# Kernel optimization log

Hardware: AMD Instinct MI355X
Metric: run time of the kernel (lower is better)

The kernel has to match this reference:

```python
import jax, jax.numpy as jnp
import numpy as np


def setup_inputs() -> dict:
    key = jax.random.key(0)
    ks = jax.random.split(key, 8)
    B, C, H, W = 4, 512, 64, 64
    Cq = C // 8
    s = 1.0 / np.sqrt(C)
    return {
        "x": jax.random.normal(ks[0], (B, C, H, W), jnp.float32),
        "Wq": jax.random.normal(ks[1], (Cq, C), jnp.float32) * s,
        "bq": jax.random.normal(ks[2], (Cq,), jnp.float32) * 0.01,
        "Wk": jax.random.normal(ks[3], (Cq, C), jnp.float32) * s,
        "bk": jax.random.normal(ks[4], (Cq,), jnp.float32) * 0.01,
        "Wv": jax.random.normal(ks[5], (C, C), jnp.float32) * s,
        "bv": jax.random.normal(ks[6], (C,), jnp.float32) * 0.01,
        "gamma": jax.random.normal(ks[7], (1,), jnp.float32),
    }


def reference(x, Wq, bq, Wk, bk, Wv, bv, gamma):
    B, C, H, W = x.shape
    N = H * W
    xf = x.reshape(B, C, N)  # flatten spatial; 1x1 conv == channel matmul
    q = jnp.einsum('oc,bcn->bon', Wq, xf) + bq[None, :, None]  # [B, C/8, N]
    k = jnp.einsum('oc,bcn->bon', Wk, xf) + bk[None, :, None]  # [B, C/8, N]
    v = jnp.einsum('oc,bcn->bon', Wv, xf) + bv[None, :, None]  # [B, C, N]
    energy = jnp.einsum('bdi,bdj->bij', q, k)                  # [B, N, N] (no scaling, as original)
    attention = jax.nn.softmax(energy, axis=-1)
    out = jnp.einsum('bcj,bij->bci', v, attention)             # bmm(v, att^T)
    out = out.reshape(B, C, H, W)
    return gamma[0] * out + x
```

## Files before the change

kernel.cpp:

```cpp
#include <hip/hip_runtime.h>


typedef float    f32x2 __attribute__((ext_vector_type(2)));
typedef float    f32x4 __attribute__((ext_vector_type(4)));
typedef _Float16 f16x4 __attribute__((ext_vector_type(4)));
typedef _Float16 f16x8 __attribute__((ext_vector_type(8)));
typedef short    bf16x8 __attribute__((ext_vector_type(8)));
typedef unsigned short u16x8 __attribute__((ext_vector_type(8)));

#define MFMA_F16(a, b, c)  __builtin_amdgcn_mfma_f32_16x16x32_f16((a), (b), (c), 0, 0, 0)
#define MFMA_BF16(a, b, c) __builtin_amdgcn_mfma_f32_16x16x32_bf16((a), (b), (c), 0, 0, 0)

__device__ __forceinline__ unsigned short bf16_rne(float f) {
    unsigned u = __builtin_bit_cast(unsigned, f);
    u += 0x7FFFu + ((u >> 16) & 1u);
    return (unsigned short)(u >> 16);
}
__device__ __forceinline__ float bf16_f(unsigned short h) {
    unsigned u = (unsigned)h << 16;
    return __builtin_bit_cast(float, u);
}

__device__ __forceinline__ void gload_lds16(const void* g, void* l) {
    __builtin_amdgcn_global_load_lds(
        (const __attribute__((address_space(1))) unsigned int*)g,
        (__attribute__((address_space(3))) unsigned int*)l, 16, 0, 0);
}

#define BARRIER_LGKM() do {                                   \
    asm volatile("s_waitcnt lgkmcnt(0)" ::: "memory");        \
    __builtin_amdgcn_s_barrier();                             \
    asm volatile("" ::: "memory");                            \
} while (0)

#define VM_WAIT8() do {                                       \
    asm volatile("s_waitcnt vmcnt(8)" ::: "memory");          \
    __builtin_amdgcn_sched_barrier(0);                        \
} while (0)
#define VM_WAIT0() do {                                       \
    asm volatile("s_waitcnt vmcnt(0)" ::: "memory");          \
    __builtin_amdgcn_sched_barrier(0);                        \
} while (0)

constexpr int BB = 4, CCH = 512, NS = 4096;

__global__ void prep_kernel(
    const float* __restrict__ Wq, const float* __restrict__ Wk,
    const float* __restrict__ Wv,
    _Float16* __restrict__ Wqh, _Float16* __restrict__ Wkh,
    _Float16* __restrict__ Wvh)
{
    const int idx = blockIdx.x * 256 + threadIdx.x;
    {
        f32x4 v = *(const f32x4*)&Wv[(size_t)idx * 4];
        f16x4 o;
#pragma unroll
        for (int e = 0; e < 4; ++e) o[e] = (_Float16)v[e];
        *(f16x4*)&Wvh[(size_t)idx * 4] = o;
    }
    if (idx < 8192) {
        f32x4 q = *(const f32x4*)&Wq[(size_t)idx * 4];
        f32x4 k = *(const f32x4*)&Wk[(size_t)idx * 4];
        f16x4 qo, ko;
#pragma unroll
        for (int e = 0; e < 4; ++e) { qo[e] = (_Float16)q[e]; ko[e] = (_Float16)k[e]; }
        *(f16x4*)&Wqh[(size_t)idx * 4] = qo;
        *(f16x4*)&Wkh[(size_t)idx * 4] = ko;
    }
}

__global__ __launch_bounds__(512, 4) void proj_kernel(
    const float* __restrict__ x,
    const _Float16* __restrict__ Wqh, const _Float16* __restrict__ Wkh,
    const _Float16* __restrict__ Wvh,
    const float* __restrict__ bq, const float* __restrict__ bk,
    const float* __restrict__ bv,
    _Float16* __restrict__ qws, _Float16* __restrict__ kws,
    unsigned short* __restrict__ vws)
{
    const int t = threadIdx.x, lane = t & 63, w = t >> 6;
    const int l15 = lane & 15, l4 = lane >> 4;
    const int b  = blockIdx.x >> 7;
    const int n0 = (blockIdx.x & 127) * 32;
    const float* xb = x + (size_t)b * CCH * NS;

    __shared__ _Float16 xt[32][32];

    f32x4 accv[4][2];
    f32x4 accq[2];
#pragma unroll
    for (int a = 0; a < 4; ++a)
#pragma unroll
        for (int n = 0; n < 2; ++n)
#pragma unroll
            for (int r = 0; r < 4; ++r) accv[a][n][r] = 0.f;
#pragma unroll
    for (int n = 0; n < 2; ++n)
#pragma unroll
        for (int r = 0; r < 4; ++r) accq[n][r] = 0.f;

    const _Float16* Wh = (w < 4) ? Wqh : Wkh;
    const int oq0 = (w & 3) * 16;
    const int stg_c = t >> 4;
    const int stg_n = (t & 15) * 2;

    f32x2 xv = *(const f32x2*)&xb[(size_t)stg_c * NS + n0 + stg_n];

    for (int cc = 0; cc < 16; ++cc) {
#pragma unroll
        for (int u = 0; u < 2; ++u) {
            const int row = stg_n + u;
            const int bcol = stg_c * 2;
            const int sw = (((bcol >> 4) ^ (row & 3)) << 4) | (bcol & 15);
            *(_Float16*)((char*)&xt[0][0] + row * 64 + sw) = (_Float16)xv[u];
        }
        BARRIER_LGKM();

        f16x8 bh[2];
#pragma unroll
        for (int nf = 0; nf < 2; ++nf) {
            const int r = nf * 16 + l15;
            bh[nf] = *(const f16x8*)((char*)&xt[0][0] + r * 64 + ((l4 ^ (r & 3)) << 4));
        }
        const int c8 = cc * 32 + l4 * 8;

        const int ccn = (cc + 1) & 15;
        xv = *(const f32x2*)&xb[(size_t)(ccn * 32 + stg_c) * NS + n0 + stg_n];

#pragma unroll
        for (int af = 0; af < 4; ++af) {
            f16x8 ah = *(const f16x8*)&Wvh[(size_t)(w * 64 + af * 16 + l15) * CCH + c8];
#pragma unroll
            for (int nf = 0; nf < 2; ++nf)
                accv[af][nf] = MFMA_F16(ah, bh[nf], accv[af][nf]);
        }
        {
            f16x8 ah = *(const f16x8*)&Wh[(size_t)(oq0 + l15) * CCH + c8];
#pragma unroll
            for (int nf = 0; nf < 2; ++nf)
                accq[nf] = MFMA_F16(ah, bh[nf], accq[nf]);
        }
        BARRIER_LGKM();
    }

#pragma unroll
    for (int af = 0; af < 4; ++af) {
#pragma unroll
        for (int r = 0; r < 4; ++r) {
            const int o = w * 64 + af * 16 + l4 * 4 + r;
            const float bias = bv[o];
#pragma unroll
            for (int nf = 0; nf < 2; ++nf) {
                const int n = n0 + nf * 16 + l15;
                vws[(size_t)(b * CCH + o) * NS + n] = bf16_rne(accv[af][nf][r] + bias);
            }
        }
    }
    {
        _Float16* oT = (w < 4) ? qws : kws;
        const float* bqk = (w < 4) ? bq : bk;
        float bias[4];
#pragma unroll
        for (int r = 0; r < 4; ++r) bias[r] = bqk[oq0 + l4 * 4 + r];
#pragma unroll
        for (int nf = 0; nf < 2; ++nf) {
            const int n = n0 + nf * 16 + l15;
            f16x4 hv;
#pragma unroll
            for (int r = 0; r < 4; ++r) hv[r] = (_Float16)(accq[nf][r] + bias[r]);
            *(f16x4*)&oT[((size_t)(b * NS + n)) * 64 + oq0 + l4 * 4] = hv;
        }
    }
}

__global__ __launch_bounds__(256, 4) void qk_kernel(
    const _Float16* __restrict__ qws, const _Float16* __restrict__ kws,
    unsigned short* __restrict__ Pws, float* __restrict__ lws2, int b0)
{
    const int t = threadIdx.x, lane = t & 63, w = t >> 6;
    const int l15 = lane & 15, l4 = lane >> 4;
    const int pb = blockIdx.x >> 8;
    const int b  = b0 + pb;
    const int r255 = blockIdx.x & 255;
    const int i0 = (r255 >> 1) * 32;
    const int jh = r255 & 1;
    const int jbase = jh * 2048;

    __shared__ unsigned short Pt[2][32][128];

    f16x8 qa[2][2];
#pragma unroll
    for (int f = 0; f < 2; ++f)
#pragma unroll
        for (int ds = 0; ds < 2; ++ds)
            qa[f][ds] = *(const f16x8*)&qws[((size_t)(b * NS + i0 + f * 16 + l15)) * 64 + ds * 32 + l4 * 8];

    const _Float16* kb = kws + (size_t)b * NS * 64;
    f16x8 kf[2][2];
#pragma unroll
    for (int jf = 0; jf < 2; ++jf)
#pragma unroll
        for (int ds = 0; ds < 2; ++ds)
            kf[jf][ds] = *(const f16x8*)&kb[(size_t)(jbase + w * 32 + jf * 16 + l15) * 64 + ds * 32 + l4 * 8];

    const int wrow = t >> 3, wg = t & 7;
    const int offA = wrow * 256 + ((wg       ^ (wrow & 7)) * 16);
    const int offB = wrow * 256 + (((wg + 8) ^ (wrow & 7)) * 16);
    unsigned short* Pgrow = Pws + ((size_t)pb * NS + i0 + wrow) * NS + jbase;
    float lacc = 0.f;

    for (int jt = 0; jt < 16; ++jt) {
        const int buf = jt & 1;
        f32x4 e[2][2];
#pragma unroll
        for (int f = 0; f < 2; ++f)
#pragma unroll
            for (int jf = 0; jf < 2; ++jf)
#pragma unroll
                for (int r = 0; r < 4; ++r) e[f][jf][r] = 0.f;
#pragma unroll
        for (int ds = 0; ds < 2; ++ds)
#pragma unroll
            for (int f = 0; f < 2; ++f)
#pragma unroll
                for (int jf = 0; jf < 2; ++jf)
                    e[f][jf] = MFMA_F16(qa[f][ds], kf[jf][ds], e[f][jf]);

        const int jn = jbase + (((jt + 1) & 15) * 128);
#pragma unroll
        for (int jf = 0; jf < 2; ++jf)
#pragma unroll
            for (int ds = 0; ds < 2; ++ds)
                kf[jf][ds] = *(const f16x8*)&kb[(size_t)(jn + w * 32 + jf * 16 + l15) * 64 + ds * 32 + l4 * 8];

        char* pbase = (char*)&Pt[buf][0][0];
#pragma unroll
        for (int f = 0; f < 2; ++f)
#pragma unroll
            for (int jf = 0; jf < 2; ++jf) {
                const int col = w * 32 + jf * 16 + l15;
#pragma unroll
                for (int r = 0; r < 4; ++r) {
                    const int row = f * 16 + l4 * 4 + r;
                    const unsigned short us = bf16_rne(__expf(e[f][jf][r]));
                    *(unsigned short*)(pbase + row * 256 +
                        (((col >> 3) ^ (row & 7)) * 16) + (col & 7) * 2) = us;
                }
            }
        BARRIER_LGKM();

        {
            char* base = (char*)&Pt[buf][0][0];
            u16x8 va = *(const u16x8*)(base + offA);
            u16x8 vb = *(const u16x8*)(base + offB);
#pragma unroll
            for (int e2 = 0; e2 < 8; ++e2)
                lacc += bf16_f((unsigned short)va[e2]) + bf16_f((unsigned short)vb[e2]);
            *(u16x8*)&Pgrow[jt * 128 + wg * 8]      = va;
            *(u16x8*)&Pgrow[jt * 128 + wg * 8 + 64] = vb;
        }
    }

    lacc += __shfl_xor(lacc, 1);
    lacc += __shfl_xor(lacc, 2);
    lacc += __shfl_xor(lacc, 4);
    if (wg == 0) lws2[((size_t)jh * BB + b) * NS + i0 + wrow] = lacc;
}

__global__ __launch_bounds__(256, 2) void pv_kernel(
    const unsigned short* __restrict__ Pws, const unsigned short* __restrict__ vws,
    const float* __restrict__ lws2, const float* __restrict__ x,
    const float* __restrict__ gamma, float* __restrict__ out, int b0, int cpx)
{
    const int t = threadIdx.x, lane = t & 63, w = t >> 6;
    const int l15 = lane & 15, l4 = lane >> 4;
    const int bid = (int)blockIdx.x;
    const int swzid = (bid & 7) * cpx + (bid >> 3);
    const int pb = swzid >> 7;
    const int b  = b0 + pb;
    const int r7 = swzid & 127;
    const int in = r7 >> 2, cm = r7 & 3;
    const int wr = w >> 1, wc = w & 1;

    __shared__ unsigned short Vt[2][128][64];
    __shared__ unsigned short Pt2[2][128][64];

    const int srow = w * 8 + (lane >> 3);
    const int sg   = (lane & 7) ^ (srow & 7);
    const unsigned short* gV = vws + ((size_t)(b * CCH + cm * 128 + srow)) * NS + sg * 8;
    const unsigned short* gP = Pws + ((size_t)(pb * NS + in * 128 + srow)) * NS + sg * 8;

    f32x4 acc[4][4];
#pragma unroll
    for (int m = 0; m < 4; ++m)
#pragma unroll
        for (int n = 0; n < 4; ++n)
#pragma unroll
            for (int r = 0; r < 4; ++r) acc[m][n][r] = 0.f;

    int offa[2][4], offb[2][4];
#pragma unroll
    for (int kk = 0; kk < 2; ++kk) {
        const int g = (kk * 4 + l4) ^ (l15 & 7);
#pragma unroll
        for (int m = 0; m < 4; ++m) {
            offa[kk][m] = (wr * 64 + m * 16 + l15) * 128 + g * 16;
            offb[kk][m] = (wc * 64 + m * 16 + l15) * 128 + g * 16;
        }
    }

#define PV_STAGE(kt, buf) do {                                                  \
    const unsigned short* _gV = gV + (size_t)(kt) * 64;                         \
    const unsigned short* _gP = gP + (size_t)(kt) * 64;                         \
    char* _lV = (char*)&Vt[buf][0][0]  + w * 1024;                              \
    char* _lP = (char*)&Pt2[buf][0][0] + w * 1024;                              \
    _Pragma("unroll")                                                           \
    for (int q = 0; q < 4; ++q) {                                               \
        gload_lds16(_gV + (size_t)q * 32 * NS, _lV + q * 4096);                 \
        gload_lds16(_gP + (size_t)q * 32 * NS, _lP + q * 4096);                 \
    }                                                                           \
} while (0)

#define PV_COMPUTE(buf) do {                                                    \
    __builtin_amdgcn_s_setprio(1);                                              \
    _Pragma("unroll")                                                           \
    for (int kk = 0; kk < 2; ++kk) {                                            \
        bf16x8 a[4], bfr[4];                                                    \
        _Pragma("unroll")                                                       \
        for (int m = 0; m < 4; ++m) {                                           \
            a[m]   = *(const bf16x8*)((char*)&Vt[buf][0][0]  + offa[kk][m]);    \
            bfr[m] = *(const bf16x8*)((char*)&Pt2[buf][0][0] + offb[kk][m]);    \
        }                                                                       \
        _Pragma("unroll")                                                       \
        for (int m = 0; m < 4; ++m)                                             \
            _Pragma("unroll")                                                   \
            for (int n = 0; n < 4; ++n)                                         \
                acc[m][n] = MFMA_BF16(a[m], bfr[n], acc[m][n]);                 \
    }                                                                           \
    __builtin_amdgcn_s_setprio(0);                                              \
} while (0)

    PV_STAGE(0, 0);
    for (int kt = 0; kt < 62; kt += 2) {
        PV_STAGE(kt + 1, 1);
        VM_WAIT8();
        __builtin_amdgcn_s_barrier();
        PV_COMPUTE(0);
        BARRIER_LGKM();
        PV_STAGE(kt + 2, 0);
        VM_WAIT8();
        __builtin_amdgcn_s_barrier();
        PV_COMPUTE(1);
        BARRIER_LGKM();
    }
    PV_STAGE(63, 1);
    VM_WAIT8();
    __builtin_amdgcn_s_barrier();
    PV_COMPUTE(0);
    BARRIER_LGKM();
    VM_WAIT0();
    __builtin_amdgcn_s_barrier();
    PV_COMPUTE(1);

#undef PV_STAGE
#undef PV_COMPUTE

    const float gm = gamma[0];
    float linv[4];
#pragma unroll
    for (int n = 0; n < 4; ++n) {
        const int i = in * 128 + wc * 64 + n * 16 + l15;
        linv[n] = 1.f / (lws2[(size_t)b * NS + i] +
                         lws2[((size_t)BB + b) * NS + i]);
    }
#pragma unroll
    for (int m = 0; m < 4; ++m) {
#pragma unroll
        for (int r = 0; r < 4; ++r) {
            const int c = cm * 128 + wr * 64 + m * 16 + l4 * 4 + r;
            const float* xr = x + ((size_t)(b * CCH + c)) * NS;
            float* orow = out + ((size_t)(b * CCH + c)) * NS;
#pragma unroll
            for (int n = 0; n < 4; ++n) {
                const int i = in * 128 + wc * 64 + n * 16 + l15;
                orow[i] = gm * acc[m][n][r] * linv[n] + xr[i];
            }
        }
    }
}

extern "C" void kernel_launch(void* const* d_in, const int* in_sizes, int n_in,
                              void* d_out, int out_size, void* d_ws, size_t ws_size,
                              hipStream_t stream)
{
    const float* x     = (const float*)d_in[0];
    const float* Wq    = (const float*)d_in[1];
    const float* bq    = (const float*)d_in[2];
    const float* Wk    = (const float*)d_in[3];
    const float* bk    = (const float*)d_in[4];
    const float* Wv    = (const float*)d_in[5];
    const float* bv    = (const float*)d_in[6];
    const float* gamma = (const float*)d_in[7];
    float* out = (float*)d_out;

    char* p = (char*)d_ws;
    size_t off = 0;
    auto take = [&](size_t bytes) { char* r = p + off; off += (bytes + 255) & ~(size_t)255; return r; };
    _Float16* qws       = (_Float16*)take((size_t)BB * NS * 64 * 2);
    _Float16* kws       = (_Float16*)take((size_t)BB * NS * 64 * 2);
    unsigned short* vws = (unsigned short*)take((size_t)BB * CCH * NS * 2);
    _Float16* Wvh       = (_Float16*)take((size_t)CCH * CCH * 2);
    _Float16* Wqh       = (_Float16*)take((size_t)64 * CCH * 2);
    _Float16* Wkh       = (_Float16*)take((size_t)64 * CCH * 2);
    float* lws2         = (float*)take((size_t)2 * BB * NS * 4);
    unsigned short* Pws = (unsigned short*)(p + off);

    const size_t P_PER_B = (size_t)NS * NS * 2;
    size_t avail = (ws_size > off) ? (ws_size - off) : 0;
    int nb = (int)(avail / P_PER_B);
    if (nb >= 4) nb = 4; else if (nb >= 2) nb = 2; else nb = 1;

    prep_kernel<<<256, 256, 0, stream>>>(Wq, Wk, Wv, Wqh, Wkh, Wvh);
    proj_kernel<<<512, 512, 0, stream>>>(x, Wqh, Wkh, Wvh, bq, bk, bv,
                                         qws, kws, vws);
    for (int b0 = 0; b0 < BB; b0 += nb) {
        const int nbb = (b0 + nb <= BB) ? nb : (BB - b0);
        qk_kernel<<<nbb * 256, 256, 0, stream>>>(qws, kws, Pws, lws2, b0);
        pv_kernel<<<nbb * 128, 256, 0, stream>>>(Pws, vws, lws2, x, gamma, out,
                                                 b0, (nbb * 128) >> 3);
    }
}
```

Baseline: 163.7 us.

## Double-buffer projection staging and make QK tile writes per-wave without block barriers

```diff
diff --git a/kernel.cpp b/kernel.cpp
--- a/kernel.cpp
+++ b/kernel.cpp
@@ -84,7 +84,7 @@
     const int n0 = (blockIdx.x & 127) * 32;
     const float* xb = x + (size_t)b * CCH * NS;
 
-    __shared__ _Float16 xt[32][32];
+    __shared__ _Float16 xt[2][32][64];
 
     f32x4 accv[4][2];
     f32x4 accq[2];
@@ -101,47 +101,57 @@
 
     const _Float16* Wh = (w < 4) ? Wqh : Wkh;
     const int oq0 = (w & 3) * 16;
-    const int stg_c = t >> 4;
-    const int stg_n = (t & 15) * 2;
-
-    f32x2 xv = *(const f32x2*)&xb[(size_t)stg_c * NS + n0 + stg_n];
-
-    for (int cc = 0; cc < 16; ++cc) {
-#pragma unroll
-        for (int u = 0; u < 2; ++u) {
-            const int row = stg_n + u;
-            const int bcol = stg_c * 2;
-            const int sw = (((bcol >> 4) ^ (row & 3)) << 4) | (bcol & 15);
-            *(_Float16*)((char*)&xt[0][0] + row * 64 + sw) = (_Float16)xv[u];
+    const int stg_c = t >> 3;
+    const int stg_n = (t & 7) * 4;
+
+#define PROJ_STAGE(B) do {                                                     \
+    char* xb_ = (char*)xt + (B) * 4096;                                        \
+    _Pragma("unroll")                                                          \
+    for (int u = 0; u < 4; ++u) {                                              \
+        const int row = stg_n + u;                                             \
+        const int g = ((stg_c >> 3) ^ (row & 7) ^ (((row >> 3) & 3) << 1)) & 7;\
+        *(_Float16*)(xb_ + row * 128 + (g << 4) + (stg_c & 7) * 2)             \
+            = (_Float16)xv[u];                                                 \
+    }                                                                          \
+} while (0)
+
+    f32x4 xv = *(const f32x4*)&xb[(size_t)stg_c * NS + n0 + stg_n];
+    PROJ_STAGE(0);
+    xv = *(const f32x4*)&xb[(size_t)(64 + stg_c) * NS + n0 + stg_n];
+    BARRIER_LGKM();
+
+    for (int cc = 0; cc < 8; ++cc) {
+        const int buf = cc & 1;
+        f16x8 bh[2][2];
+#pragma unroll
+        for (int nf = 0; nf < 2; ++nf)
+#pragma unroll
+            for (int ds = 0; ds < 2; ++ds) {
+                const int row = nf * 16 + l15;
+                const int g = ((ds * 4 + l4) ^ (row & 7) ^ (((row >> 3) & 3) << 1)) & 7;
+                bh[nf][ds] = *(const f16x8*)((char*)xt + buf * 4096 + row * 128 + (g << 4));
+            }
+        PROJ_STAGE(buf ^ 1);
+        xv = *(const f32x4*)&xb[(size_t)((((cc + 2) & 7) * 64) + stg_c) * NS + n0 + stg_n];
+
+#pragma unroll
+        for (int ds = 0; ds < 2; ++ds) {
+            const int c8 = cc * 64 + ds * 32 + l4 * 8;
+            f16x8 ahq = *(const f16x8*)&Wh[(size_t)(oq0 + l15) * CCH + c8];
+#pragma unroll
+            for (int af = 0; af < 4; ++af) {
+                f16x8 ah = *(const f16x8*)&Wvh[(size_t)(w * 64 + af * 16 + l15) * CCH + c8];
+#pragma unroll
+                for (int nf = 0; nf < 2; ++nf)
+                    accv[af][nf] = MFMA_F16(ah, bh[nf][ds], accv[af][nf]);
+            }
+#pragma unroll
+            for (int nf = 0; nf < 2; ++nf)
+                accq[nf] = MFMA_F16(ahq, bh[nf][ds], accq[nf]);
         }
         BARRIER_LGKM();
-
-        f16x8 bh[2];
-#pragma unroll
-        for (int nf = 0; nf < 2; ++nf) {
-            const int r = nf * 16 + l15;
-            bh[nf] = *(const f16x8*)((char*)&xt[0][0] + r * 64 + ((l4 ^ (r & 3)) << 4));
-        }
-        const int c8 = cc * 32 + l4 * 8;
-
-        const int ccn = (cc + 1) & 15;
-        xv = *(const f32x2*)&xb[(size_t)(ccn * 32 + stg_c) * NS + n0 + stg_n];
-
-#pragma unroll
-        for (int af = 0; af < 4; ++af) {
-            f16x8 ah = *(const f16x8*)&Wvh[(size_t)(w * 64 + af * 16 + l15) * CCH + c8];
-#pragma unroll
-            for (int nf = 0; nf < 2; ++nf)
-                accv[af][nf] = MFMA_F16(ah, bh[nf], accv[af][nf]);
-        }
-        {
-            f16x8 ah = *(const f16x8*)&Wh[(size_t)(oq0 + l15) * CCH + c8];
-#pragma unroll
-            for (int nf = 0; nf < 2; ++nf)
-                accq[nf] = MFMA_F16(ah, bh[nf], accq[nf]);
-        }
-        BARRIER_LGKM();
-    }
+    }
+#undef PROJ_STAGE
 
 #pragma unroll
     for (int af = 0; af < 4; ++af) {
@@ -184,9 +194,10 @@
     const int r255 = blockIdx.x & 255;
     const int i0 = (r255 >> 1) * 32;
     const int jh = r255 & 1;
-    const int jbase = jh * 2048;
-
-    __shared__ unsigned short Pt[2][32][128];
+    const int jw = jh * 2048 + w * 512;
+
+    __shared__ unsigned short Pt[4][32][32];
+    __shared__ float Lred[4][32];
 
     f16x8 qa[2][2];
 #pragma unroll
@@ -201,16 +212,22 @@
     for (int jf = 0; jf < 2; ++jf)
 #pragma unroll
         for (int ds = 0; ds < 2; ++ds)
-            kf[jf][ds] = *(const f16x8*)&kb[(size_t)(jbase + w * 32 + jf * 16 + l15) * 64 + ds * 32 + l4 * 8];
-
-    const int wrow = t >> 3, wg = t & 7;
-    const int offA = wrow * 256 + ((wg       ^ (wrow & 7)) * 16);
-    const int offB = wrow * 256 + (((wg + 8) ^ (wrow & 7)) * 16);
-    unsigned short* Pgrow = Pws + ((size_t)pb * NS + i0 + wrow) * NS + jbase;
-    float lacc = 0.f;
+            kf[jf][ds] = *(const f16x8*)&kb[(size_t)(jw + jf * 16 + l15) * 64 + ds * 32 + l4 * 8];
+
+    f32x4 lacc[2];
+#pragma unroll
+    for (int f = 0; f < 2; ++f)
+#pragma unroll
+        for (int r = 0; r < 4; ++r) lacc[f][r] = 0.f;
+
+    char* wbase = (char*)&Pt[w][0][0];
+    const int rrow = lane >> 1, h = lane & 1;
+    const int rsw = (rrow & 3) ^ (((rrow >> 2) & 1) << 1);
+    const int rg0 = (((2 * h)     ^ rsw) & 3) << 4;
+    const int rg1 = (((2 * h + 1) ^ rsw) & 3) << 4;
+    unsigned short* Pg = Pws + ((size_t)pb * NS + i0 + rrow) * NS + jw + h * 16;
 
     for (int jt = 0; jt < 16; ++jt) {
-        const int buf = jt & 1;
         f32x4 e[2][2];
 #pragma unroll
         for (int f = 0; f < 2; ++f)
@@ -226,45 +243,56 @@
                 for (int jf = 0; jf < 2; ++jf)
                     e[f][jf] = MFMA_F16(qa[f][ds], kf[jf][ds], e[f][jf]);
 
-        const int jn = jbase + (((jt + 1) & 15) * 128);
+        const int jn = jw + ((jt + 1) & 15) * 32;
 #pragma unroll
         for (int jf = 0; jf < 2; ++jf)
 #pragma unroll
             for (int ds = 0; ds < 2; ++ds)
-                kf[jf][ds] = *(const f16x8*)&kb[(size_t)(jn + w * 32 + jf * 16 + l15) * 64 + ds * 32 + l4 * 8];
-
-        char* pbase = (char*)&Pt[buf][0][0];
+                kf[jf][ds] = *(const f16x8*)&kb[(size_t)(jn + jf * 16 + l15) * 64 + ds * 32 + l4 * 8];
+
 #pragma unroll
         for (int f = 0; f < 2; ++f)
 #pragma unroll
             for (int jf = 0; jf < 2; ++jf) {
-                const int col = w * 32 + jf * 16 + l15;
+                const int col = jf * 16 + l15;
+                const int cg = col >> 3;
 #pragma unroll
                 for (int r = 0; r < 4; ++r) {
                     const int row = f * 16 + l4 * 4 + r;
                     const unsigned short us = bf16_rne(__expf(e[f][jf][r]));
-                    *(unsigned short*)(pbase + row * 256 +
-                        (((col >> 3) ^ (row & 7)) * 16) + (col & 7) * 2) = us;
+                    lacc[f][r] += bf16_f(us);
+                    const int g = ((cg ^ (row & 3) ^ (((row >> 2) & 1) << 1)) & 3) << 4;
+                    *(unsigned short*)(wbase + row * 64 + g + (col & 7) * 2) = us;
                 }
             }
-        BARRIER_LGKM();
+
+        asm volatile("s_waitcnt lgkmcnt(0)" ::: "memory");
+        __builtin_amdgcn_sched_barrier(0);
 
         {
-            char* base = (char*)&Pt[buf][0][0];
-            u16x8 va = *(const u16x8*)(base + offA);
-            u16x8 vb = *(const u16x8*)(base + offB);
-#pragma unroll
-            for (int e2 = 0; e2 < 8; ++e2)
-                lacc += bf16_f((unsigned short)va[e2]) + bf16_f((unsigned short)vb[e2]);
-            *(u16x8*)&Pgrow[jt * 128 + wg * 8]      = va;
-            *(u16x8*)&Pgrow[jt * 128 + wg * 8 + 64] = vb;
-        }
-    }
-
-    lacc += __shfl_xor(lacc, 1);
-    lacc += __shfl_xor(lacc, 2);
-    lacc += __shfl_xor(lacc, 4);
-    if (wg == 0) lws2[((size_t)jh * BB + b) * NS + i0 + wrow] = lacc;
+            u16x8 va = *(const u16x8*)(wbase + rrow * 64 + rg0);
+            u16x8 vb = *(const u16x8*)(wbase + rrow * 64 + rg1);
+            *(u16x8*)&Pg[jt * 32]     = va;
+            *(u16x8*)&Pg[jt * 32 + 8] = vb;
+        }
+    }
+
+#pragma unroll
+    for (int f = 0; f < 2; ++f)
+#pragma unroll
+        for (int r = 0; r < 4; ++r) {
+            float v = lacc[f][r];
+            v += __shfl_xor(v, 1);
+            v += __shfl_xor(v, 2);
+            v += __shfl_xor(v, 4);
+            v += __shfl_xor(v, 8);
+            if (l15 == 0) Lred[w][f * 16 + l4 * 4 + r] = v;
+        }
+    __syncthreads();
+    if (t < 32) {
+        const float s = Lred[0][t] + Lred[1][t] + Lred[2][t] + Lred[3][t];
+        lws2[((size_t)jh * BB + b) * NS + i0 + t] = s;
+    }
 }
 
 __global__ __launch_bounds__(256, 2) void pv_kernel(
```

New measurement: 167.9 us. 1.03x slower.

## Replace projection kernel with transposed-x fp16 staging and tiled LDS-pipelined GEMM

Applied to the files above, without the earlier changes.

```diff
diff --git a/kernel.cpp b/kernel.cpp
--- a/kernel.cpp
+++ b/kernel.cpp
@@ -46,9 +46,7 @@
 
 __global__ void prep_kernel(
     const float* __restrict__ Wq, const float* __restrict__ Wk,
-    const float* __restrict__ Wv,
-    _Float16* __restrict__ Wqh, _Float16* __restrict__ Wkh,
-    _Float16* __restrict__ Wvh)
+    const float* __restrict__ Wv, _Float16* __restrict__ Wall)
 {
     const int idx = blockIdx.x * 256 + threadIdx.x;
     {
@@ -56,7 +54,7 @@
         f16x4 o;
 #pragma unroll
         for (int e = 0; e < 4; ++e) o[e] = (_Float16)v[e];
-        *(f16x4*)&Wvh[(size_t)idx * 4] = o;
+        *(f16x4*)&Wall[(size_t)128 * 512 + idx * 4] = o;
     }
     if (idx < 8192) {
         f32x4 q = *(const f32x4*)&Wq[(size_t)idx * 4];
@@ -64,15 +62,41 @@
         f16x4 qo, ko;
 #pragma unroll
         for (int e = 0; e < 4; ++e) { qo[e] = (_Float16)q[e]; ko[e] = (_Float16)k[e]; }
-        *(f16x4*)&Wqh[(size_t)idx * 4] = qo;
-        *(f16x4*)&Wkh[(size_t)idx * 4] = ko;
-    }
-}
-
-__global__ __launch_bounds__(512, 4) void proj_kernel(
-    const float* __restrict__ x,
-    const _Float16* __restrict__ Wqh, const _Float16* __restrict__ Wkh,
-    const _Float16* __restrict__ Wvh,
+        *(f16x4*)&Wall[(size_t)idx * 4] = qo;
+        *(f16x4*)&Wall[(size_t)64 * 512 + idx * 4] = ko;
+    }
+}
+
+__global__ __launch_bounds__(256, 4) void xT_kernel(
+    const float* __restrict__ x, _Float16* __restrict__ xT)
+{
+    const int t = threadIdx.x;
+    const int bid = (int)blockIdx.x;
+    const int nt = bid & 63;
+    const int ct = (bid >> 6) & 7;
+    const int b  = bid >> 9;
+    const int c0 = ct * 64, n0 = nt * 64;
+
+    __shared__ _Float16 tl[64][72];
+
+    const float* xb = x + ((size_t)(b * CCH + c0)) * NS + n0;
+    const int rr = t >> 4, cc4 = (t & 15) * 4;
+#pragma unroll
+    for (int s = 0; s < 4; ++s) {
+        f32x4 v = *(const f32x4*)&xb[(size_t)(rr + s * 16) * NS + cc4];
+#pragma unroll
+        for (int e = 0; e < 4; ++e)
+            tl[cc4 + e][rr + s * 16] = (_Float16)v[e];
+    }
+    __syncthreads();
+    const int nr = t >> 2, cg = (t & 3) * 16;
+    _Float16* dst = xT + ((size_t)(b * NS) + n0 + nr) * 512 + c0 + cg;
+    *(u16x8*)dst       = *(const u16x8*)&tl[nr][cg];
+    *(u16x8*)(dst + 8) = *(const u16x8*)&tl[nr][cg + 8];
+}
+
+__global__ __launch_bounds__(256, 2) void proj_gemm(
+    const _Float16* __restrict__ Wall, const _Float16* __restrict__ xT,
     const float* __restrict__ bq, const float* __restrict__ bk,
     const float* __restrict__ bv,
     _Float16* __restrict__ qws, _Float16* __restrict__ kws,
@@ -80,95 +104,128 @@
 {
     const int t = threadIdx.x, lane = t & 63, w = t >> 6;
     const int l15 = lane & 15, l4 = lane >> 4;
-    const int b  = blockIdx.x >> 7;
-    const int n0 = (blockIdx.x & 127) * 32;
-    const float* xb = x + (size_t)b * CCH * NS;
-
-    __shared__ _Float16 xt[32][32];
-
-    f32x4 accv[4][2];
-    f32x4 accq[2];
-#pragma unroll
-    for (int a = 0; a < 4; ++a)
-#pragma unroll
-        for (int n = 0; n < 2; ++n)
-#pragma unroll
-            for (int r = 0; r < 4; ++r) accv[a][n][r] = 0.f;
-#pragma unroll
-    for (int n = 0; n < 2; ++n)
-#pragma unroll
-        for (int r = 0; r < 4; ++r) accq[n][r] = 0.f;
-
-    const _Float16* Wh = (w < 4) ? Wqh : Wkh;
-    const int oq0 = (w & 3) * 16;
-    const int stg_c = t >> 4;
-    const int stg_n = (t & 15) * 2;
-
-    f32x2 xv = *(const f32x2*)&xb[(size_t)stg_c * NS + n0 + stg_n];
-
-    for (int cc = 0; cc < 16; ++cc) {
-#pragma unroll
-        for (int u = 0; u < 2; ++u) {
-            const int row = stg_n + u;
-            const int bcol = stg_c * 2;
-            const int sw = (((bcol >> 4) ^ (row & 3)) << 4) | (bcol & 15);
-            *(_Float16*)((char*)&xt[0][0] + row * 64 + sw) = (_Float16)xv[u];
-        }
+    const int bid = (int)blockIdx.x;
+    const int swzid = (bid & 7) * 80 + (bid >> 3);
+    const int b  = swzid / 160;
+    const int rem = swzid - b * 160;
+    const int nt = rem / 5;
+    const int mt = rem - nt * 5;
+    const int wr = w >> 1, wc = w & 1;
+
+    __shared__ unsigned short At[2][128][64];
+    __shared__ unsigned short Bt[2][128][64];
+
+    const int srow = w * 8 + (lane >> 3);
+    const int sg   = (lane & 7) ^ (srow & 7);
+    const _Float16* gA = Wall + ((size_t)(mt * 128 + srow)) * 512 + sg * 8;
+    const _Float16* gB = xT + ((size_t)(b * NS + nt * 128 + srow)) * 512 + sg * 8;
+
+    f32x4 acc[4][4];
+#pragma unroll
+    for (int m = 0; m < 4; ++m)
+#pragma unroll
+        for (int n = 0; n < 4; ++n)
+#pragma unroll
+            for (int r = 0; r < 4; ++r) acc[m][n][r] = 0.f;
+
+    int offa[2][4], offb[2][4];
+#pragma unroll
+    for (int kk = 0; kk < 2; ++kk) {
+        const int g = (kk * 4 + l4) ^ (l15 & 7);
+#pragma unroll
+        for (int m = 0; m < 4; ++m) {
+            offa[kk][m] = (wr * 64 + m * 16 + l15) * 128 + g * 16;
+            offb[kk][m] = (wc * 64 + m * 16 + l15) * 128 + g * 16;
+        }
+    }
+
+#define PG_STAGE(kt, buf) do {                                                  \
+    const _Float16* _gA = gA + (size_t)(kt) * 64;                               \
+    const _Float16* _gB = gB + (size_t)(kt) * 64;                               \
+    char* _lA = (char*)&At[buf][0][0] + w * 1024;                               \
+    char* _lB = (char*)&Bt[buf][0][0] + w * 1024;                               \
+    _Pragma("unroll")                                                           \
+    for (int q = 0; q < 4; ++q) {                                               \
+        gload_lds16(_gA + (size_t)q * 32 * 512, _lA + q * 4096);                \
+        gload_lds16(_gB + (size_t)q * 32 * 512, _lB + q * 4096);                \
+    }                                                                           \
+} while (0)
+
+#define PG_COMPUTE(buf) do {                                                    \
+    __builtin_amdgcn_s_setprio(1);                                              \
+    _Pragma("unroll")                                                           \
+    for (int kk = 0; kk < 2; ++kk) {                                            \
+        f16x8 a[4], bb[4];                                                      \
+        _Pragma("unroll")                                                       \
+        for (int m = 0; m < 4; ++m) {                                           \
+            a[m]  = *(const f16x8*)((char*)&At[buf][0][0] + offa[kk][m]);       \
+            bb[m] = *(const f16x8*)((char*)&Bt[buf][0][0] + offb[kk][m]);       \
+        }                                                                       \
+        _Pragma("unroll")                                                       \
+        for (int m = 0; m < 4; ++m)                                             \
+            _Pragma("unroll")                                                   \
+            for (int n = 0; n < 4; ++n)                                         \
+                acc[m][n] = MFMA_F16(a[m], bb[n], acc[m][n]);                   \
+    }                                                                           \
+    __builtin_amdgcn_s_setprio(0);                                              \
+} while (0)
+
+    PG_STAGE(0, 0);
+    for (int kt = 0; kt < 6; kt += 2) {
+        PG_STAGE(kt + 1, 1);
+        VM_WAIT8();
+        __builtin_amdgcn_s_barrier();
+        PG_COMPUTE(0);
         BARRIER_LGKM();
-
-        f16x8 bh[2];
-#pragma unroll
-        for (int nf = 0; nf < 2; ++nf) {
-            const int r = nf * 16 + l15;
-            bh[nf] = *(const f16x8*)((char*)&xt[0][0] + r * 64 + ((l4 ^ (r & 3)) << 4));
-        }
-        const int c8 = cc * 32 + l4 * 8;
-
-        const int ccn = (cc + 1) & 15;
-        xv = *(const f32x2*)&xb[(size_t)(ccn * 32 + stg_c) * NS + n0 + stg_n];
-
-#pragma unroll
-        for (int af = 0; af < 4; ++af) {
-            f16x8 ah = *(const f16x8*)&Wvh[(size_t)(w * 64 + af * 16 + l15) * CCH + c8];
-#pragma unroll
-            for (int nf = 0; nf < 2; ++nf)
-                accv[af][nf] = MFMA_F16(ah, bh[nf], accv[af][nf]);
-        }
-        {
-            f16x8 ah = *(const f16x8*)&Wh[(size_t)(oq0 + l15) * CCH + c8];
-#pragma unroll
-            for (int nf = 0; nf < 2; ++nf)
-                accq[nf] = MFMA_F16(ah, bh[nf], accq[nf]);
-        }
+        PG_STAGE(kt + 2, 0);
+        VM_WAIT8();
+        __builtin_amdgcn_s_barrier();
+        PG_COMPUTE(1);
         BARRIER_LGKM();
     }
-
-#pragma unroll
-    for (int af = 0; af < 4; ++af) {
-#pragma unroll
-        for (int r = 0; r < 4; ++r) {
-            const int o = w * 64 + af * 16 + l4 * 4 + r;
-            const float bias = bv[o];
-#pragma unroll
-            for (int nf = 0; nf < 2; ++nf) {
-                const int n = n0 + nf * 16 + l15;
-                vws[(size_t)(b * CCH + o) * NS + n] = bf16_rne(accv[af][nf][r] + bias);
+    PG_STAGE(7, 1);
+    VM_WAIT8();
+    __builtin_amdgcn_s_barrier();
+    PG_COMPUTE(0);
+    BARRIER_LGKM();
+    VM_WAIT0();
+    __builtin_amdgcn_s_barrier();
+    PG_COMPUTE(1);
+
+#undef PG_STAGE
+#undef PG_COMPUTE
+
+    if (mt == 0) {
+        _Float16* dst = (wr == 0) ? qws : kws;
+        const float* bias = (wr == 0) ? bq : bk;
+#pragma unroll
+        for (int m = 0; m < 4; ++m) {
+#pragma unroll
+            for (int r = 0; r < 4; ++r) {
+                const int oo = m * 16 + l4 * 4 + r;
+                const float bi = bias[oo];
+#pragma unroll
+                for (int n = 0; n < 4; ++n) {
+                    const int i = nt * 128 + wc * 64 + n * 16 + l15;
+                    dst[((size_t)(b * NS + i)) * 64 + oo] =
+                        (_Float16)(acc[m][n][r] + bi);
+                }
             }
         }
-    }
-    {
-        _Float16* oT = (w < 4) ? qws : kws;
-        const float* bqk = (w < 4) ? bq : bk;
-        float bias[4];
-#pragma unroll
-        for (int r = 0; r < 4; ++r) bias[r] = bqk[oq0 + l4 * 4 + r];
-#pragma unroll
-        for (int nf = 0; nf < 2; ++nf) {
-            const int n = n0 + nf * 16 + l15;
-            f16x4 hv;
-#pragma unroll
-            for (int r = 0; r < 4; ++r) hv[r] = (_Float16)(accq[nf][r] + bias[r]);
-            *(f16x4*)&oT[((size_t)(b * NS + n)) * 64 + oq0 + l4 * 4] = hv;
+    } else {
+#pragma unroll
+        for (int m = 0; m < 4; ++m) {
+#pragma unroll
+            for (int r = 0; r < 4; ++r) {
+                const int c = (mt - 1) * 128 + wr * 64 + m * 16 + l4 * 4 + r;
+                const float bi = bv[c];
+                unsigned short* orow = vws + ((size_t)(b * CCH + c)) * NS;
+#pragma unroll
+                for (int n = 0; n < 4; ++n) {
+                    const int i = nt * 128 + wc * 64 + n * 16 + l15;
+                    orow[i] = bf16_rne(acc[m][n][r] + bi);
+                }
+            }
         }
     }
 }
@@ -409,9 +466,8 @@
     _Float16* qws       = (_Float16*)take((size_t)BB * NS * 64 * 2);
     _Float16* kws       = (_Float16*)take((size_t)BB * NS * 64 * 2);
     unsigned short* vws = (unsigned short*)take((size_t)BB * CCH * NS * 2);
-    _Float16* Wvh       = (_Float16*)take((size_t)CCH * CCH * 2);
-    _Float16* Wqh       = (_Float16*)take((size_t)64 * CCH * 2);
-    _Float16* Wkh       = (_Float16*)take((size_t)64 * CCH * 2);
+    _Float16* Wall      = (_Float16*)take((size_t)640 * 512 * 2);
+    _Float16* xT        = (_Float16*)take((size_t)BB * NS * 512 * 2);
     float* lws2         = (float*)take((size_t)2 * BB * NS * 4);
     unsigned short* Pws = (unsigned short*)(p + off);
 
@@ -420,9 +476,9 @@
     int nb = (int)(avail / P_PER_B);
     if (nb >= 4) nb = 4; else if (nb >= 2) nb = 2; else nb = 1;
 
-    prep_kernel<<<256, 256, 0, stream>>>(Wq, Wk, Wv, Wqh, Wkh, Wvh);
-    proj_kernel<<<512, 512, 0, stream>>>(x, Wqh, Wkh, Wvh, bq, bk, bv,
-                                         qws, kws, vws);
+    prep_kernel<<<256, 256, 0, stream>>>(Wq, Wk, Wv, Wall);
+    xT_kernel<<<2048, 256, 0, stream>>>(x, xT);
+    proj_gemm<<<640, 256, 0, stream>>>(Wall, xT, bq, bk, bv, qws, kws, vws);
     for (int b0 = 0; b0 < BB; b0 += nb) {
         const int nbb = (b0 + nb <= BB) ? nb : (BB - b0);
         qk_kernel<<<nbb * 256, 256, 0, stream>>>(qws, kws, Pws, lws2, b0);
```

New measurement: 153.0 us. 6.5% less time.
